# Performance work log

Hardware: AMD Instinct MI355X
Metric: run time of the kernel (lower is better)

The kernel has to match this reference:

```python
import jax, jax.numpy as jnp
import numpy as np

N, K = 8192, 133
N_LAYERS = 6
HID = 64
# mmpose RealNVP coupling masks: [0,1],[1,0] repeated 3 times
MASK = jnp.array([[0.0, 1.0], [1.0, 0.0]] * 3, dtype=jnp.float32)  # [6,2]


def _mlp(x, w1, b1, w2, b2, w3, b3):
    # x: [P,2] -> [P,2]; LeakyReLU slope 0.01 (torch default)
    h = jax.nn.leaky_relu(x @ w1.T + b1, 0.01)
    h = jax.nn.leaky_relu(h @ w2.T + b2, 0.01)
    return h @ w3.T + b3


def _flow_log_prob(x, s_w1, s_b1, s_w2, s_b2, s_w3, s_b3,
                   t_w1, t_b1, t_w2, t_b2, t_w3, t_b3):
    # RealNVP backward pass: x -> z, accumulating log-det Jacobian
    z = x
    log_det = jnp.zeros(x.shape[0], x.dtype)
    for i in reversed(range(N_LAYERS)):
        m = MASK[i]
        z_ = m * z
        s = jnp.tanh(_mlp(z_, s_w1[i], s_b1[i], s_w2[i], s_b2[i], s_w3[i], s_b3[i])) * (1.0 - m)
        t = _mlp(z_, t_w1[i], t_b1[i], t_w2[i], t_b2[i], t_w3[i], t_b3[i]) * (1.0 - m)
        z = (1.0 - m) * (z - t) * jnp.exp(-s) + z_
        log_det = log_det - s.sum(axis=1)
    # standard 2D normal prior log-prob
    prior_lp = -0.5 * jnp.sum(z * z, axis=1) - jnp.log(2.0 * jnp.pi)
    return prior_lp + log_det


def setup_inputs() -> dict:
    key = jax.random.key(0)
    ks = jax.random.split(key, 16)
    inp = {
        'pred': jax.random.normal(ks[0], (N, K, 4), dtype=jnp.float32),
        'target': jax.random.normal(ks[1], (N, K, 2), dtype=jnp.float32),
        'target_weight': jax.random.uniform(ks[2], (N, K), dtype=jnp.float32),
    }
    dims = [(HID, 2), (HID,), (HID, HID), (HID,), (2, HID), (2,)]
    names = ['w1', 'b1', 'w2', 'b2', 'w3', 'b3']
    kidx = 3
    for pfx in ('s', 't'):
        for nm, d in zip(names, dims):
            inp[f'{pfx}_{nm}'] = 0.1 * jax.random.normal(ks[kidx], (N_LAYERS,) + d, dtype=jnp.float32)
            kidx += 1
    return inp


def reference(pred, target, target_weight,
              s_w1, s_b1, s_w2, s_b2, s_w3, s_b3,
              t_w1, t_b1, t_w2, t_b2, t_w3, t_b3):
    miu = pred[:, :, :2]
    sigma = jnp.sqrt(jnp.abs(pred[:, :, 2:4]))  # sigmoid=False
    error = (miu - target) / (sigma + 1e-9)  # [N,K,2]
    log_phi = _flow_log_prob(error.reshape(-1, 2),
                             s_w1, s_b1, s_w2, s_b2, s_w3, s_b3,
                             t_w1, t_b1, t_w2, t_b2, t_w3, t_b3)
    log_phi = log_phi.reshape(pred.shape[0], pred.shape[1], 1)
    log_sigma = jnp.log(sigma)
    nf_loss = log_sigma - log_phi  # [N,K,2]
    # residual=True, q_distribution='laplace'
    loss_q = jnp.log(sigma * 2.0) + jnp.abs(error)
    loss = nf_loss + loss_q
    loss = loss * target_weight[:, :, None]  # use_target_weight=True
    loss = loss / pred.shape[0]  # size_average=True: divide by len(loss)=N
    return loss.sum()
```

## Files before the change

kernel.cpp:

```cpp
#include <hip/hip_runtime.h>

typedef _Float16 hfrag_t __attribute__((ext_vector_type(8)));
typedef _Float16 h2_t    __attribute__((ext_vector_type(2)));
typedef __attribute__((ext_vector_type(4))) float    f4_t;
typedef __attribute__((ext_vector_type(4))) unsigned u4_t;

#define LOG_2PI   1.8378770664093453f
#define TWO_LOG2  1.3862943611198906f
#define T_TILES   4
#define BLOCK     256
#define PTS_BLK   256
#define ZCLAMP    30000.0f

__device__ __forceinline__ h2_t pkh2(float a, float b) {
  return __builtin_bit_cast(h2_t, __builtin_amdgcn_cvt_pkrtz(a, b));
}
__device__ __forceinline__ unsigned pku(float a, float b) {
  return __builtin_bit_cast(unsigned, pkh2(a, b));
}
__device__ __forceinline__ h2_t leaky2(h2_t h) {
  h2_t t = h * (h2_t){(_Float16)0.01f, (_Float16)0.01f};
  return __builtin_elementwise_max(h, t);
}
__device__ __forceinline__ float dot2h(h2_t a, h2_t b, float c) {
  return __builtin_amdgcn_fdot2(a, b, c, false);
}

__device__ __forceinline__ void stage_layer(u4_t* afr, const float* sW2, const float* tW2,
                                            int layer, int tid) {
  #pragma unroll
  for (int it = 0; it < 4; ++it) {
    int idx = tid + it * BLOCK;
    int l = idx & 63, f = (idx >> 6) & 7, m = (idx >> 9) & 1;
    int n = f & 3, q = f >> 2;
    int row = 16 * n + (l & 15), kb = 32 * q + 8 * (l >> 4);
    const float* src = (m ? tW2 : sW2) + layer * 4096 + row * 64 + kb;
    float4 a = *(const float4*)src;
    float4 b = *(const float4*)(src + 4);
    afr[(m * 8 + f) * 64 + l] =
        (u4_t){pku(a.x, a.y), pku(a.z, a.w), pku(b.x, b.y), pku(b.z, b.w)};
  }
}

__global__ __launch_bounds__(BLOCK)
void ihll_kernel(
    const float* __restrict__ pred, const float* __restrict__ targ, const float* __restrict__ twp,
    const float* __restrict__ sW1, const float* __restrict__ sB1, const float* __restrict__ sW2,
    const float* __restrict__ sB2, const float* __restrict__ sW3, const float* __restrict__ sB3,
    const float* __restrict__ tW1, const float* __restrict__ tB1, const float* __restrict__ tW2,
    const float* __restrict__ tB2, const float* __restrict__ tW3, const float* __restrict__ tB3,
    float* __restrict__ out, int M) {
  __shared__ u4_t     afr[2 * 8 * 64];
  __shared__ unsigned c1h[6][2][32];
  __shared__ unsigned b1h[6][2][32];
  __shared__ unsigned w3h[6][2][4][8];
  __shared__ float    b2s[6][2][64];
  __shared__ float    wsum[4];

  const int tid  = threadIdx.x;
  const int lane = tid & 63, wave = tid >> 6;
  const int pr   = lane & 15, g = lane >> 4;
  const int pbase = blockIdx.x * PTS_BLK;

  for (int idx = tid; idx < 384; idx += BLOCK) {
    int i = idx >> 6, r = idx & 63, m = r >> 5, jp = r & 31;
    int jo = i & 1, jm = jo ^ 1;
    const float* w1 = m ? tW1 : sW1;  const float* b1 = m ? tB1 : sB1;
    c1h[i][m][jp] = pku(w1[i * 128 + 4 * jp + jm], w1[i * 128 + 4 * jp + 2 + jm]);
    b1h[i][m][jp] = pku(b1[i * 64 + 2 * jp], b1[i * 64 + 2 * jp + 1]);
  }
  for (int idx = tid; idx < 384; idx += BLOCK) {
    int i = idx >> 6, r = idx & 63, m = r >> 5, c = r & 31;
    int gg = c >> 3, c2 = c & 7, n = c2 >> 1, jj = c2 & 1;
    int jo = i & 1;
    const float* w3 = m ? tW3 : sW3;
    int row = 16 * n + 4 * gg + 2 * jj;
    w3h[i][m][gg][c2] = pku(w3[i * 128 + jo * 64 + row], w3[i * 128 + jo * 64 + row + 1]);
  }
  for (int idx = tid; idx < 768; idx += BLOCK) {
    int i = idx >> 7, r = idx & 127, m = r >> 6, j = r & 63;
    const float* b2 = m ? tB2 : sB2;
    b2s[i][m][j] = b2[i * 64 + j];
  }

  float z0[T_TILES], z1[T_TILES], ld[T_TILES], pre0[T_TILES];
  #pragma unroll
  for (int t = 0; t < T_TILES; ++t) {
    int P = pbase + wave * 64 + t * 16 + pr;
    float e0 = 0.f, e1 = 0.f;
    if (P < M) {
      float4 p4 = ((const float4*)pred)[P];
      float2 t2 = ((const float2*)targ)[P];
      float s0 = sqrtf(fabsf(p4.z)), s1 = sqrtf(fabsf(p4.w));
      e0 = (p4.x - t2.x) / (s0 + 1e-9f);
      e1 = (p4.y - t2.y) / (s1 + 1e-9f);
    }
    z0[t] = e0; z1[t] = e1; ld[t] = 0.f; pre0[t] = 0.f;
  }
  stage_layer(afr, sW2, tW2, 5, tid);
  __syncthreads();

  #pragma unroll 1
  for (int li = 0; li < 6; ++li) {
    const int i = 5 - li;
    const int jo = i & 1;
    const bool upd0 = (jo == 0);
    const float b3s = sB3[i * 2 + jo];
    const float b3t = tB3[i * 2 + jo];

    h2_t zz[T_TILES];
    #pragma unroll
    for (int t = 0; t < T_TILES; ++t) {
      float zin = upd0 ? z1[t] : z0[t];
      zin = fmaxf(fminf(zin, ZCLAMP), -ZCLAMP);
      zz[t] = pkh2(zin, zin);
    }

    #pragma unroll
    for (int m = 0; m < 2; ++m) {
      u4_t af[8];
      #pragma unroll
      for (int f = 0; f < 8; ++f)
        af[f] = afr[(m * 8 + f) * 64 + lane];
      h2_t c1q[8], b1q[8];
      *(u4_t*)&c1q[0] = *(const u4_t*)&c1h[i][m][4 * g];
      *(u4_t*)&c1q[4] = *(const u4_t*)&c1h[i][m][16 + 4 * g];
      *(u4_t*)&b1q[0] = *(const u4_t*)&b1h[i][m][4 * g];
      *(u4_t*)&b1q[4] = *(const u4_t*)&b1h[i][m][16 + 4 * g];
      h2_t w3q[8];
      *(u4_t*)&w3q[0] = *(const u4_t*)&w3h[i][m][g][0];
      *(u4_t*)&w3q[4] = *(const u4_t*)&w3h[i][m][g][4];
      f4_t b2q[4];
      #pragma unroll
      for (int n = 0; n < 4; ++n)
        b2q[n] = *(const f4_t*)&b2s[i][m][n * 16 + 4 * g];

      #pragma unroll
      for (int t = 0; t < T_TILES; ++t) {
        f4_t acc[4];
        #pragma unroll
        for (int q = 0; q < 2; ++q) {
          h2_t hh[4];
          #pragma unroll
          for (int e = 0; e < 4; ++e)
            hh[e] = leaky2(c1q[q * 4 + e] * zz[t] + b1q[q * 4 + e]);
          hfrag_t B = __builtin_bit_cast(hfrag_t, hh);
          #pragma unroll
          for (int n = 0; n < 4; ++n) {
            f4_t c = (q == 0) ? b2q[n] : acc[n];
            acc[n] = __builtin_amdgcn_mfma_f32_16x16x32_f16(
                __builtin_bit_cast(hfrag_t, af[q * 4 + n]), B, c, 0, 0, 0);
          }
        }
        float pa_ = 0.f, pb_ = 0.f;
        #pragma unroll
        for (int n = 0; n < 4; ++n) {
          h2_t a01 = leaky2(pkh2(acc[n][0], acc[n][1]));
          h2_t a23 = leaky2(pkh2(acc[n][2], acc[n][3]));
          if (n < 2) {
            pa_ = dot2h(a01, w3q[2 * n], pa_);
            pa_ = dot2h(a23, w3q[2 * n + 1], pa_);
          } else {
            pb_ = dot2h(a01, w3q[2 * n], pb_);
            pb_ = dot2h(a23, w3q[2 * n + 1], pb_);
          }
        }
        float pt = pa_ + pb_;
        pt += __shfl_xor(pt, 16);
        pt += __shfl_xor(pt, 32);

        if (m == 0) {
          pre0[t] = pt;
        } else {
          float sv = 1.f - 2.f / (__expf(2.f * (pre0[t] + b3s)) + 1.f);
          float tv = pt + b3t;
          float zo = upd0 ? z0[t] : z1[t];
          float zn = (zo - tv) * __expf(-sv);
          if (upd0) z0[t] = zn; else z1[t] = zn;
          ld[t] -= sv;
        }
      }
    }
    __syncthreads();
    if (li < 5) {
      stage_layer(afr, sW2, tW2, i - 1, tid);
      __syncthreads();
    }
  }

  float csum = 0.f;
  #pragma unroll
  for (int t = 0; t < T_TILES; ++t) {
    int P = pbase + wave * 64 + t * 16 + pr;
    if (P < M) {
      float4 p4 = ((const float4*)pred)[P];
      float2 t2 = ((const float2*)targ)[P];
      float w   = twp[P];
      float s0 = sqrtf(fabsf(p4.z)), s1 = sqrtf(fabsf(p4.w));
      float e0 = (p4.x - t2.x) / (s0 + 1e-9f);
      float e1 = (p4.y - t2.y) / (s1 + 1e-9f);
      float bs = 2.f * (logf(s0) + logf(s1)) + TWO_LOG2 + fabsf(e0) + fabsf(e1);
      float prior = -0.5f * (z0[t] * z0[t] + z1[t] * z1[t]) - LOG_2PI;
      float lphi  = prior + ld[t];
      csum += (bs - 2.f * lphi) * w;
    }
  }
  #pragma unroll
  for (int off = 1; off <= 32; off <<= 1)
    csum += __shfl_xor(csum, off);
  if (lane == 0) wsum[wave] = csum;
  __syncthreads();
  if (tid == 0) {
    float tot = wsum[0] + wsum[1] + wsum[2] + wsum[3];
    atomicAdd(out, tot * (1.0f / 32768.0f));
  }
}

extern "C" void kernel_launch(void* const* d_in, const int* in_sizes, int n_in,
                              void* d_out, int out_size, void* d_ws, size_t ws_size,
                              hipStream_t stream) {
  const float* pred = (const float*)d_in[0];
  const float* targ = (const float*)d_in[1];
  const float* twp  = (const float*)d_in[2];
  const float* sW1 = (const float*)d_in[3];  const float* sB1 = (const float*)d_in[4];
  const float* sW2 = (const float*)d_in[5];  const float* sB2 = (const float*)d_in[6];
  const float* sW3 = (const float*)d_in[7];  const float* sB3 = (const float*)d_in[8];
  const float* tW1 = (const float*)d_in[9];  const float* tB1 = (const float*)d_in[10];
  const float* tW2 = (const float*)d_in[11]; const float* tB2 = (const float*)d_in[12];
  const float* tW3 = (const float*)d_in[13]; const float* tB3 = (const float*)d_in[14];

  const int M = in_sizes[2];
  const int blocks = (M + PTS_BLK - 1) / PTS_BLK;

  hipMemsetAsync(d_out, 0, sizeof(float), stream);
  hipLaunchKernelGGL(ihll_kernel, dim3(blocks), dim3(BLOCK), 0, stream,
                     pred, targ, twp, sW1, sB1, sW2, sB2, sW3, sB3,
                     tW1, tB1, tW2, tB2, tW3, tB3, (float*)d_out, M);
}
```

Before: 234.5 us.

## Double-buffer W2 fragment staging and prefetch next layer during compute

Result: slower. 245.0 us (+4.5%).

```diff
diff --git a/kernel.cpp b/kernel.cpp
--- a/kernel.cpp
+++ b/kernel.cpp
@@ -26,8 +26,9 @@
   return __builtin_amdgcn_fdot2(a, b, c, false);
 }
 
-__device__ __forceinline__ void stage_layer(u4_t* afr, const float* sW2, const float* tW2,
-                                            int layer, int tid) {
+__device__ __forceinline__ void stage_load(float4* sa, float4* sb,
+                                           const float* sW2, const float* tW2,
+                                           int layer, int tid) {
   #pragma unroll
   for (int it = 0; it < 4; ++it) {
     int idx = tid + it * BLOCK;
@@ -35,8 +36,17 @@
     int n = f & 3, q = f >> 2;
     int row = 16 * n + (l & 15), kb = 32 * q + 8 * (l >> 4);
     const float* src = (m ? tW2 : sW2) + layer * 4096 + row * 64 + kb;
-    float4 a = *(const float4*)src;
-    float4 b = *(const float4*)(src + 4);
+    sa[it] = *(const float4*)src;
+    sb[it] = *(const float4*)(src + 4);
+  }
+}
+__device__ __forceinline__ void stage_store(u4_t* afr, const float4* sa, const float4* sb,
+                                            int tid) {
+  #pragma unroll
+  for (int it = 0; it < 4; ++it) {
+    int idx = tid + it * BLOCK;
+    int l = idx & 63, f = (idx >> 6) & 7, m = (idx >> 9) & 1;
+    float4 a = sa[it], b = sb[it];
     afr[(m * 8 + f) * 64 + l] =
         (u4_t){pku(a.x, a.y), pku(a.z, a.w), pku(b.x, b.y), pku(b.z, b.w)};
   }
@@ -50,17 +60,19 @@
     const float* __restrict__ tW1, const float* __restrict__ tB1, const float* __restrict__ tW2,
     const float* __restrict__ tB2, const float* __restrict__ tW3, const float* __restrict__ tB3,
     float* __restrict__ out, int M) {
-  __shared__ u4_t     afr[2 * 8 * 64];
+  __shared__ u4_t     afr[2][2 * 8 * 64];
   __shared__ unsigned c1h[6][2][32];
   __shared__ unsigned b1h[6][2][32];
   __shared__ unsigned w3h[6][2][4][8];
   __shared__ float    b2s[6][2][64];
   __shared__ float    wsum[4];
+  __shared__ float    pad[512];
 
   const int tid  = threadIdx.x;
   const int lane = tid & 63, wave = tid >> 6;
   const int pr   = lane & 15, g = lane >> 4;
   const int pbase = blockIdx.x * PTS_BLK;
+  if (M == 0) pad[tid] = (float)tid;
 
   for (int idx = tid; idx < 384; idx += BLOCK) {
     int i = idx >> 6, r = idx & 63, m = r >> 5, jp = r & 31;
@@ -97,16 +109,24 @@
     }
     z0[t] = e0; z1[t] = e1; ld[t] = 0.f; pre0[t] = 0.f;
   }
-  stage_layer(afr, sW2, tW2, 5, tid);
+  {
+    float4 sa[4], sb[4];
+    stage_load(sa, sb, sW2, tW2, 5, tid);
+    stage_store(afr[0], sa, sb, tid);
+  }
   __syncthreads();
 
   #pragma unroll 1
   for (int li = 0; li < 6; ++li) {
     const int i = 5 - li;
+    const int cur = li & 1;
     const int jo = i & 1;
     const bool upd0 = (jo == 0);
     const float b3s = sB3[i * 2 + jo];
     const float b3t = tB3[i * 2 + jo];
+
+    float4 sa[4], sb[4];
+    if (li < 5) stage_load(sa, sb, sW2, tW2, i - 1, tid);
 
     h2_t zz[T_TILES];
     #pragma unroll
@@ -121,7 +141,7 @@
       u4_t af[8];
       #pragma unroll
       for (int f = 0; f < 8; ++f)
-        af[f] = afr[(m * 8 + f) * 64 + lane];
+        af[f] = afr[cur][(m * 8 + f) * 64 + lane];
       h2_t c1q[8], b1q[8];
       *(u4_t*)&c1q[0] = *(const u4_t*)&c1h[i][m][4 * g];
       *(u4_t*)&c1q[4] = *(const u4_t*)&c1h[i][m][16 + 4 * g];
@@ -181,11 +201,8 @@
         }
       }
     }
+    if (li < 5) stage_store(afr[cur ^ 1], sa, sb, tid);
     __syncthreads();
-    if (li < 5) {
-      stage_layer(afr, sW2, tW2, i - 1, tid);
-      __syncthreads();
-    }
   }
 
   float csum = 0.f;
```

## Load W2 MFMA fragments directly from global memory, drop LDS staging

Applied to the files above, without the earlier changes.

Measured after the change: 402.3 us. +71.6%, slower.

```diff
diff --git a/kernel.cpp b/kernel.cpp
--- a/kernel.cpp
+++ b/kernel.cpp
@@ -24,22 +24,6 @@
 }
 __device__ __forceinline__ float dot2h(h2_t a, h2_t b, float c) {
   return __builtin_amdgcn_fdot2(a, b, c, false);
-}
-
-__device__ __forceinline__ void stage_layer(u4_t* afr, const float* sW2, const float* tW2,
-                                            int layer, int tid) {
-  #pragma unroll
-  for (int it = 0; it < 4; ++it) {
-    int idx = tid + it * BLOCK;
-    int l = idx & 63, f = (idx >> 6) & 7, m = (idx >> 9) & 1;
-    int n = f & 3, q = f >> 2;
-    int row = 16 * n + (l & 15), kb = 32 * q + 8 * (l >> 4);
-    const float* src = (m ? tW2 : sW2) + layer * 4096 + row * 64 + kb;
-    float4 a = *(const float4*)src;
-    float4 b = *(const float4*)(src + 4);
-    afr[(m * 8 + f) * 64 + l] =
-        (u4_t){pku(a.x, a.y), pku(a.z, a.w), pku(b.x, b.y), pku(b.z, b.w)};
-  }
 }
 
 __global__ __launch_bounds__(BLOCK)
@@ -50,17 +34,18 @@
     const float* __restrict__ tW1, const float* __restrict__ tB1, const float* __restrict__ tW2,
     const float* __restrict__ tB2, const float* __restrict__ tW3, const float* __restrict__ tB3,
     float* __restrict__ out, int M) {
-  __shared__ u4_t     afr[2 * 8 * 64];
   __shared__ unsigned c1h[6][2][32];
   __shared__ unsigned b1h[6][2][32];
   __shared__ unsigned w3h[6][2][4][8];
   __shared__ float    b2s[6][2][64];
   __shared__ float    wsum[4];
+  __shared__ float    pad[7548];
 
   const int tid  = threadIdx.x;
   const int lane = tid & 63, wave = tid >> 6;
   const int pr   = lane & 15, g = lane >> 4;
   const int pbase = blockIdx.x * PTS_BLK;
+  if (M == 0) pad[tid] = (float)tid;
 
   for (int idx = tid; idx < 384; idx += BLOCK) {
     int i = idx >> 6, r = idx & 63, m = r >> 5, jp = r & 31;
@@ -97,7 +82,6 @@
     }
     z0[t] = e0; z1[t] = e1; ld[t] = 0.f; pre0[t] = 0.f;
   }
-  stage_layer(afr, sW2, tW2, 5, tid);
   __syncthreads();
 
   #pragma unroll 1
@@ -118,10 +102,16 @@
 
     #pragma unroll
     for (int m = 0; m < 2; ++m) {
+      const float* wsrc = (m ? tW2 : sW2) + i * 4096;
       u4_t af[8];
       #pragma unroll
-      for (int f = 0; f < 8; ++f)
-        af[f] = afr[(m * 8 + f) * 64 + lane];
+      for (int f = 0; f < 8; ++f) {
+        int n = f & 3, q = f >> 2;
+        const float* s = wsrc + (16 * n + pr) * 64 + 32 * q + 8 * g;
+        float4 a = *(const float4*)s;
+        float4 b = *(const float4*)(s + 4);
+        af[f] = (u4_t){pku(a.x, a.y), pku(a.z, a.w), pku(b.x, b.y), pku(b.z, b.w)};
+      }
       h2_t c1q[8], b1q[8];
       *(u4_t*)&c1q[0] = *(const u4_t*)&c1h[i][m][4 * g];
       *(u4_t*)&c1q[4] = *(const u4_t*)&c1h[i][m][16 + 4 * g];
@@ -181,11 +171,6 @@
         }
       }
     }
-    __syncthreads();
-    if (li < 5) {
-      stage_layer(afr, sW2, tW2, i - 1, tid);
-      __syncthreads();
-    }
   }
 
   float csum = 0.f;
```
